# Performance work log

Hardware: AMD Instinct MI355X
Metric: run time of the kernel (lower is better)

Reference implementation:

```python
import jax, jax.numpy as jnp
import numpy as np

N, E, D, ED = 100000, 500000, 64, 32
MSG_IN = 4 * D + ED + 4  # 292


def _xavier(k, fi, fo):
    lim = np.sqrt(6.0 / (fi + fo)).astype(np.float32)
    return jax.random.uniform(k, (fi, fo), jnp.float32, -lim, lim)


def mlp(x, W1, b1, W2, b2):
    return jax.nn.gelu(x @ W1 + b1, approximate=False) @ W2 + b2


def layernorm(x, g, b, eps=1e-5):
    m = jnp.mean(x, -1, keepdims=True)
    v = jnp.mean((x - m) ** 2, -1, keepdims=True)
    return (x - m) / jnp.sqrt(v + eps) * g + b


def setup_inputs() -> dict:
    key = jax.random.key(0)
    ks = jax.random.split(key, 40)
    node_u = jax.random.normal(ks[0], (N, 5), jnp.float32)
    src = jax.random.randint(ks[1], (E,), 0, N)
    dst = jax.random.randint(ks[2], (E,), 0, N)
    edge_index = jnp.stack([src, dst], 0).astype(jnp.int64)
    dxy = jax.random.normal(ks[3], (E, 2), jnp.float32) * 0.01
    r = jnp.linalg.norm(dxy, axis=-1, keepdims=True)
    edge_attr = jnp.concatenate([dxy, r], -1)
    mean_mom = jax.random.normal(ks[4], (2,), jnp.float32)
    std_mom = jax.random.uniform(ks[5], (2,), jnp.float32) + 0.5
    edge_memory = jax.random.normal(ks[6], (E, D), jnp.float32) * 0.1
    p = {}
    # phi_node: 5->64->64
    p['pn_W1'] = _xavier(ks[7], 5, D); p['pn_b1'] = jnp.zeros((D,))
    p['pn_W2'] = _xavier(ks[8], D, D); p['pn_b2'] = jnp.zeros((D,))
    # input_proj: 5->64
    p['ip_W'] = _xavier(ks[9], 5, D); p['ip_b'] = jnp.zeros((D,))
    # phi_edge: 1->32->32
    p['pe_W1'] = _xavier(ks[10], 1, ED); p['pe_b1'] = jnp.zeros((ED,))
    p['pe_W2'] = _xavier(ks[11], ED, ED); p['pe_b2'] = jnp.zeros((ED,))
    # phi_msg: 292->128->64
    p['pm_W1'] = _xavier(ks[12], MSG_IN, 128); p['pm_b1'] = jnp.zeros((128,))
    p['pm_W2'] = _xavier(ks[13], 128, D); p['pm_b2'] = jnp.zeros((D,))
    # psi_rho: 64->64->1
    p['prho_W1'] = _xavier(ks[14], D, 64); p['prho_b1'] = jnp.zeros((64,))
    p['prho_W2'] = _xavier(ks[15], 64, 1); p['prho_b2'] = jnp.zeros((1,))
    # psi_e: 64->64->1
    p['pen_W1'] = _xavier(ks[16], D, 64); p['pen_b1'] = jnp.zeros((64,))
    p['pen_W2'] = _xavier(ks[17], 64, 1); p['pen_b2'] = jnp.zeros((1,))
    # psi_rhou: 64->64->2
    p['pmu_W1'] = _xavier(ks[18], D, 64); p['pmu_b1'] = jnp.zeros((64,))
    p['pmu_W2'] = _xavier(ks[19], 64, 2); p['pmu_b2'] = jnp.zeros((2,))
    # psi_visc: 64->32->1
    p['pv_W1'] = _xavier(ks[20], D, 32); p['pv_b1'] = jnp.zeros((32,))
    p['pv_W2'] = _xavier(ks[21], 32, 1); p['pv_b2'] = jnp.zeros((1,))
    p['ln_g'] = jnp.ones((D,)); p['ln_b'] = jnp.zeros((D,))
    return dict(node_u=node_u, edge_attr=edge_attr, mean_mom=mean_mom,
                std_mom=std_mom, edge_memory=edge_memory, edge_index=edge_index, **p)


def reference(node_u, edge_attr, mean_mom, std_mom, edge_memory,
              pn_W1, pn_b1, pn_W2, pn_b2, ip_W, ip_b,
              pe_W1, pe_b1, pe_W2, pe_b2, pm_W1, pm_b1, pm_W2, pm_b2,
              prho_W1, prho_b1, prho_W2, prho_b2, pen_W1, pen_b1, pen_W2, pen_b2,
              pmu_W1, pmu_b1, pmu_W2, pmu_b2, pv_W1, pv_b1, pv_W2, pv_b2,
              ln_g, ln_b, edge_index):
    src, dst = edge_index[0], edge_index[1]
    dx, dy, r = edge_attr[:, 0:1], edge_attr[:, 1:2], edge_attr[:, 2:3]
    n = jnp.concatenate([dx, dy], -1) / (r + 1e-12)            # (E,2) unit normals
    t = jnp.stack([-n[:, 1], n[:, 0]], axis=1)                 # (E,2) tangents
    # momentum projections in physical units
    rhou_phys = node_u[:, 3:5] * std_mom + mean_mom            # (N,2)
    rs, rd = rhou_phys[src], rhou_phys[dst]
    scale = jnp.linalg.norm(std_mom) + 1e-8
    vel_proj = jnp.concatenate([
        jnp.sum(rs * n, -1, keepdims=True), jnp.sum(rs * t, -1, keepdims=True),
        jnp.sum(rd * n, -1, keepdims=True), jnp.sum(rd * t, -1, keepdims=True)], -1) / scale
    # node embeddings with residual projection
    h = mlp(node_u, pn_W1, pn_b1, pn_W2, pn_b2) + node_u @ ip_W + ip_b
    h_src, h_dst = h[src], h[dst]
    eps = mlp(r, pe_W1, pe_b1, pe_W2, pe_b2)                   # (E,32)
    msg_in = jnp.concatenate([h_src, h_dst, h_src + h_dst,
                              (h_src - h_dst) ** 2, eps, vel_proj], -1)  # (E,292)
    m = mlp(msg_in, pm_W1, pm_b1, pm_W2, pm_b2)                # (E,64)
    m = layernorm(m + edge_memory, ln_g, ln_b)
    a_rho = mlp(m, prho_W1, prho_b1, prho_W2, prho_b2)[:, 0]
    a_e = mlp(m, pen_W1, pen_b1, pen_W2, pen_b2)[:, 0]
    a_rhou = mlp(m, pmu_W1, pmu_b1, pmu_W2, pmu_b2)            # (E,2)
    alpha = jax.nn.sigmoid(mlp(m, pv_W1, pv_b1, pv_W2, pv_b2)[:, 0])[:, None]
    du = node_u[dst] - node_u[src]
    F_rho = a_rho[:, None] * n - alpha * du[:, 0:1] * n
    F_e = a_e[:, None] * n - alpha * du[:, 1:2] * n
    F_rhou = a_rhou[:, 0:1] * n + a_rhou[:, 1:2] * t - alpha * du[:, 3:5]
    return (F_rho, F_e, F_rhou, n, r[:, 0], alpha[:, 0], m)
```

## Files before the change

kernel.cpp:

```cpp
#include <hip/hip_runtime.h>
#include <math.h>

#define NN 100000
#define NE 500000

typedef short bf16x8 __attribute__((ext_vector_type(8)));
typedef float f32x4 __attribute__((ext_vector_type(4)));
typedef float f32x16 __attribute__((ext_vector_type(16)));

__device__ __forceinline__ float gelu_f(float x) {
  const float t = x * x;
  const float p = fmaf(t, 0.10294325f, 2.3022084f);
  const float E = __builtin_amdgcn_exp2f(x * p);
  const float r = __builtin_amdgcn_rcpf(E + 1.0f);
  return fmaf(-x, r, x);
}
__device__ __forceinline__ unsigned cvtpk(float lo, float hi) {
  unsigned r;
  asm("v_cvt_pk_bf16_f32 %0, %1, %2" : "=v"(r) : "v"(lo), "v"(hi));
  return r;
}
__device__ __forceinline__ short f2bf(float x) { return (short)cvtpk(x, x); }
__device__ __forceinline__ unsigned pack2(float a, float b) { return cvtpk(a, b); }
__device__ __forceinline__ float bf2f(short s) {
  unsigned u = ((unsigned)(unsigned short)s) << 16;
  return __builtin_bit_cast(float, u);
}
__device__ __forceinline__ float bf2f_lo(unsigned w) {
  return __builtin_bit_cast(float, w << 16);
}
__device__ __forceinline__ float bf2f_hi(unsigned w) {
  return __builtin_bit_cast(float, w & 0xFFFF0000u);
}

#define MFMA16(a, b, c) __builtin_amdgcn_mfma_f32_16x16x32_bf16((a), (b), (c), 0, 0, 0)
#define MFMA32(a, b, c) __builtin_amdgcn_mfma_f32_32x32x16_bf16((a), (b), (c), 0, 0, 0)

__global__ __launch_bounds__(256) void node_h_kernel(
    const float* __restrict__ node_u,
    const float* __restrict__ b1, const float* __restrict__ b2,
    const float* __restrict__ ipb,
    const short* __restrict__ W1NP, const short* __restrict__ IPNP,
    const short* __restrict__ W2NP,
    unsigned short* __restrict__ h) {
  __shared__ float sU[64 * 5];
  __shared__ short sG[64 * 72];
  const int tid = threadIdx.x;
  const int lane = tid & 63;
  const int wv = tid >> 6;
  const int l31 = lane & 31, hi = lane >> 5;
  const int mt = wv & 1, nh = wv >> 1;
  const int n0 = blockIdx.x * 64;
  const int nrem = NN - n0;

  {
    const int cnt = (nrem < 64 ? nrem : 64) * 5;
    for (int t = tid; t < cnt; t += 256) sU[t] = node_u[(size_t)n0 * 5 + t];
  }
  __syncthreads();

  const int row_node = mt * 32 + l31;
  const int col = nh * 32 + l31;
  bf16x8 au;
#pragma unroll
  for (int e = 0; e < 8; ++e)
    au[e] = (hi == 0 && e < 5) ? f2bf(sU[row_node * 5 + e]) : (short)0;
  f32x16 acc1, accip;
  const float b1v = b1[col];
  const float ipv = ipb[col] + b2[col];
#pragma unroll
  for (int reg = 0; reg < 16; ++reg) { acc1[reg] = b1v; accip[reg] = ipv; }
  acc1 = MFMA32(au, *(const bf16x8*)(W1NP + nh * 512 + lane * 8), acc1);
  accip = MFMA32(au, *(const bf16x8*)(IPNP + nh * 512 + lane * 8), accip);
#pragma unroll
  for (int reg = 0; reg < 16; ++reg) {
    const int r = mt * 32 + (reg & 3) + 8 * (reg >> 2) + 4 * hi;
    sG[r * 72 + col] = f2bf(gelu_f(acc1[reg]));
  }
  __syncthreads();

  {
    const char* arow = (const char*)sG + row_node * 144 + hi * 16;
    const short* BW = W2NP + nh * 4 * 512 + lane * 8;
    f32x16 acc = accip;
#pragma unroll
    for (int ks = 0; ks < 4; ++ks)
      acc = MFMA32(*(const bf16x8*)(arow + ks * 32),
                   *(const bf16x8*)(BW + ks * 512), acc);
#pragma unroll
    for (int reg = 0; reg < 16; ++reg) {
      const int r = mt * 32 + (reg & 3) + 8 * (reg >> 2) + 4 * hi;
      const int node = n0 + r;
      if (node < NN) h[(size_t)node * 64 + col] = (unsigned short)f2bf(acc[reg]);
    }
  }
}

__global__ __launch_bounds__(256) void prep_kernel(
    const float* __restrict__ pm_W1, const float* __restrict__ pm_b1,
    const float* __restrict__ pm_W2,
    const float* __restrict__ prho_W1, const float* __restrict__ pen_W1,
    const float* __restrict__ pmu_W1, const float* __restrict__ pv_W1,
    const float* __restrict__ prho_b1, const float* __restrict__ pen_b1,
    const float* __restrict__ pmu_b1, const float* __restrict__ pv_b1,
    const float* __restrict__ pe_W2, const float* __restrict__ pe_b2,
    const float* __restrict__ prho_W2, const float* __restrict__ pen_W2,
    const float* __restrict__ pmu_W2, const float* __restrict__ pv_W2,
    const float* __restrict__ prho_b2, const float* __restrict__ pen_b2,
    const float* __restrict__ pmu_b2, const float* __restrict__ pv_b2,
    const float* __restrict__ pn_W1, const float* __restrict__ pn_W2,
    const float* __restrict__ ip_W,
    short* __restrict__ W1P, short* __restrict__ W2P, short* __restrict__ WHP,
    float* __restrict__ HB, short* __restrict__ WOP, float* __restrict__ HB2,
    float* __restrict__ B1F, short* __restrict__ W1NP, short* __restrict__ IPNP,
    short* __restrict__ W2NP) {
  int t = blockIdx.x * 256 + threadIdx.x;
  if (t < 30720) {
    const int nt = t / 7680, rem = t % 7680;
    const int ks = rem / 512, li = rem % 512;
    const int l = li >> 3, e = li & 7;
    const int k = ks * 16 + ((l >> 5) << 3) + e;
    const int n = nt * 32 + (l & 31);
    float v = 0.0f;
    if (k < 64) v = pm_W1[k * 128 + n] + pm_W1[(128 + k) * 128 + n];
    else if (k < 128) v = pm_W1[k * 128 + n] + pm_W1[(64 + k) * 128 + n];
    else if (k < 192) v = pm_W1[(64 + k) * 128 + n];
    else if (k < 224) {
      const int i = k - 192;
      for (int j = 0; j < 32; ++j) v += pe_W2[i * 32 + j] * pm_W1[(256 + j) * 128 + n];
    } else if (k < 228) v = pm_W1[(64 + k) * 128 + n];
    W1P[t] = f2bf(v);
    return;
  }
  t -= 30720;
  if (t < 8192) {
    const int nt = t / 2048, rem = t % 2048;
    const int ks = rem / 512, li = rem % 512;
    const int l = li >> 3, e = li & 7;
    const int k = ks * 32 + ((l >> 4) << 3) + e;
    const int n = nt * 16 + (l & 15);
    W2P[t] = f2bf(pm_W2[k * 64 + n]);
    return;
  }
  t -= 8192;
  if (t < 14336) {
    const int nt = t / 2048, rem = t % 2048;
    const int ks = rem / 512, li = rem % 512;
    const int l = li >> 3, e = li & 7;
    const int k = ks * 16 + ((l >> 5) << 3) + e;
    const int col = nt * 32 + (l & 31);
    float v;
    if (col < 64) v = prho_W1[k * 64 + col];
    else if (col < 128) v = pen_W1[k * 64 + (col - 64)];
    else if (col < 192) v = pmu_W1[k * 64 + (col - 128)];
    else v = pv_W1[k * 32 + (col - 192)];
    WHP[t] = f2bf(v);
    return;
  }
  t -= 14336;
  if (t < 224) {
    HB[t] = (t < 64) ? prho_b1[t]
          : (t < 128) ? pen_b1[t - 64]
          : (t < 192) ? pmu_b1[t - 128]
          : pv_b1[t - 192];
    return;
  }
  t -= 224;
  if (t < 3584) {
    const int ks = t / 512, li = t % 512;
    const int l = li >> 3, e = li & 7;
    const int k = ks * 32 + ((l >> 4) << 3) + e;
    const int j = l & 15;
    float v = 0.0f;
    if (j == 0 && k < 64) v = prho_W2[k];
    else if (j == 1 && k >= 64 && k < 128) v = pen_W2[k - 64];
    else if (j == 2 && k >= 128 && k < 192) v = pmu_W2[(k - 128) * 2 + 0];
    else if (j == 3 && k >= 128 && k < 192) v = pmu_W2[(k - 128) * 2 + 1];
    else if (j == 4 && k >= 192 && k < 224) v = pv_W2[k - 192];
    WOP[t] = f2bf(v);
    return;
  }
  t -= 3584;
  if (t < 16) {
    HB2[t] = (t == 0) ? prho_b2[0]
           : (t == 1) ? pen_b2[0]
           : (t == 2) ? pmu_b2[0]
           : (t == 3) ? pmu_b2[1]
           : (t == 4) ? pv_b2[0] : 0.0f;
    return;
  }
  t -= 16;
  if (t < 128) {
    float v = pm_b1[t];
    for (int j = 0; j < 32; ++j) v += pe_b2[j] * pm_W1[(256 + j) * 128 + t];
    B1F[t] = v;
    return;
  }
  t -= 128;
  if (t < 1024) {
    const int nt = t / 512, li = t % 512;
    const int l = li >> 3, e = li & 7;
    const int k = ((l >> 5) << 3) + e;
    const int n = nt * 32 + (l & 31);
    W1NP[t] = (k < 5) ? f2bf(pn_W1[k * 64 + n]) : (short)0;
    return;
  }
  t -= 1024;
  if (t < 1024) {
    const int nt = t / 512, li = t % 512;
    const int l = li >> 3, e = li & 7;
    const int k = ((l >> 5) << 3) + e;
    const int n = nt * 32 + (l & 31);
    IPNP[t] = (k < 5) ? f2bf(ip_W[k * 64 + n]) : (short)0;
    return;
  }
  t -= 1024;
  if (t < 4096) {
    const int nt = t / 2048, rem = t % 2048;
    const int ks = rem / 512, li = rem % 512;
    const int l = li >> 3, e = li & 7;
    const int k = ks * 16 + ((l >> 5) << 3) + e;
    const int n = nt * 32 + (l & 31);
    W2NP[t] = f2bf(pn_W2[k * 64 + n]);
  }
}

struct EdgeArgs {
  const float *node_u, *edge_attr, *mean_mom, *std_mom, *edge_mem;
  const int* eidx;
  const float *pe_W1, *pe_b1;
  const float *B1F, *pm_b2;
  const float *ln_g, *ln_b;
  const unsigned short* h;
  const short *W1P, *W2P, *WHP, *WOP;
  const float *HB, *HB2;
  float* out;
};

#define SMS 248
#define H1S 136
#define MSR 72
#define ZST 248

#define OFF_A    0
#define OFF_AM   15872
#define OFF_SC   20480
#define OFF_SC2  21504
#define OFF_PART 22528
#define SMEM_BYTES 23040

__global__ __launch_bounds__(256, 7) void edge_kernel(EdgeArgs A) {
  __shared__ __align__(16) char smem[SMEM_BYTES];
  short* aA = (short*)(smem + OFF_A);
  short* aZ = (short*)(smem + OFF_A);
  short* aH1 = (short*)(smem + OFF_A);
  short* aM = (short*)(smem + OFF_AM);
  float* sSc = (float*)(smem + OFF_SC);
  float* sSc2 = (float*)(smem + OFF_SC2);
  float2* sPart = (float2*)(smem + OFF_PART);

  const int tid = threadIdx.x;
  const int e0 = blockIdx.x * 32;
  const int lane = tid & 63;
  const int wv = tid >> 6;
  const int l15 = lane & 15, g = lane >> 4;
  const int l31 = lane & 31, hi = lane >> 5;
  const int mt = wv & 1, nh = wv >> 1;

  if (tid < 32) {
    const int e = e0 + tid;
    const int s = A.eidx[e];
    const int d = A.eidx[NE + e];
    const float dx = A.edge_attr[e * 3 + 0];
    const float dy = A.edge_attr[e * 3 + 1];
    const float r = A.edge_attr[e * 3 + 2];
    const float inv = 1.0f / (r + 1e-12f);
    const float n0 = dx * inv, n1 = dy * inv;
    const float* us = A.node_u + (size_t)s * 5;
    const float* ud = A.node_u + (size_t)d * 5;
    const float sm0 = A.std_mom[0], sm1 = A.std_mom[1];
    const float mm0 = A.mean_mom[0], mm1 = A.mean_mom[1];
    const float rs0 = fmaf(us[3], sm0, mm0), rs1 = fmaf(us[4], sm1, mm1);
    const float rd0 = fmaf(ud[3], sm0, mm0), rd1 = fmaf(ud[4], sm1, mm1);
    const float isc = 1.0f / (sqrtf(sm0 * sm0 + sm1 * sm1) + 1e-8f);
    unsigned* vp = (unsigned*)(aA + tid * SMS + 224);
    vp[0] = pack2((rs0 * n0 + rs1 * n1) * isc, (-rs0 * n1 + rs1 * n0) * isc);
    vp[1] = pack2((rd0 * n0 + rd1 * n1) * isc, (-rd0 * n1 + rd1 * n0) * isc);
    unsigned* zp = (unsigned*)(aA + tid * SMS + 228);
#pragma unroll
    for (int z = 0; z < 6; ++z) zp[z] = 0u;
    float* st = &sSc[tid * 8];
    st[0] = n0; st[1] = n1; st[2] = r;
    st[3] = ud[0] - us[0];
    st[4] = ud[1] - us[1];
    st[5] = ud[3] - us[3];
    st[6] = ud[4] - us[4];
  }
  {
    const int i = tid & 31, eg = tid >> 5;
    const float w1 = A.pe_W1[i], b1 = A.pe_b1[i];
#pragma unroll
    for (int p = 0; p < 4; ++p) {
      const int el = eg * 4 + p;
      const float rv = A.edge_attr[(e0 + el) * 3 + 2];
      aA[el * SMS + 192 + i] = f2bf(gelu_f(fmaf(rv, w1, b1)));
    }
  }
  {
    const int c = tid & 31, eg = tid >> 5;
    int si[4], di[4];
#pragma unroll
    for (int p = 0; p < 4; ++p) {
      si[p] = A.eidx[e0 + eg * 4 + p];
      di[p] = A.eidx[NE + e0 + eg * 4 + p];
    }
    unsigned usr[4], udr[4];
#pragma unroll
    for (int p = 0; p < 4; ++p) {
      usr[p] = ((const unsigned*)(A.h + (size_t)si[p] * 64))[c];
      udr[p] = ((const unsigned*)(A.h + (size_t)di[p] * 64))[c];
    }
#pragma unroll
    for (int p = 0; p < 4; ++p) {
      const int el = eg * 4 + p;
      unsigned* rp = (unsigned*)((char*)aA + el * (SMS * 2));
      rp[c] = usr[p];
      rp[32 + c] = udr[p];
      const float s0 = bf2f_lo(usr[p]), s1 = bf2f_hi(usr[p]);
      const float d0 = bf2f_lo(udr[p]), d1 = bf2f_hi(udr[p]);
      const float q0 = s0 - d0, q1 = s1 - d1;
      rp[64 + c] = pack2(q0 * q0, q1 * q1);
    }
  }
  __syncthreads();

  unsigned h1pk[8];
  {
    const char* arow = (const char*)aA + l31 * (SMS * 2) + hi * 16;
    const short* BW = A.W1P + wv * 15 * 512 + lane * 8;
    f32x16 acc = {0.f, 0.f, 0.f, 0.f, 0.f, 0.f, 0.f, 0.f,
                  0.f, 0.f, 0.f, 0.f, 0.f, 0.f, 0.f, 0.f};
    for (int ks = 0; ks < 15; ++ks) {
      acc = MFMA32(*(const bf16x8*)(arow + ks * 32),
                   *(const bf16x8*)(BW + ks * 512), acc);
    }
    const float bb = A.B1F[wv * 32 + l31];
#pragma unroll
    for (int r8 = 0; r8 < 8; ++r8)
      h1pk[r8] = pack2(gelu_f(acc[2 * r8] + bb), gelu_f(acc[2 * r8 + 1] + bb));
  }
  __syncthreads();

  {
    const int col = wv * 32 + l31;
#pragma unroll
    for (int r8 = 0; r8 < 8; ++r8) {
      const int reg = 2 * r8;
      const int row = (reg & 3) + 8 * (reg >> 2) + 4 * hi;
      aH1[row * H1S + col] = (short)h1pk[r8];
      aH1[(row + 1) * H1S + col] = (short)(h1pk[r8] >> 16);
    }
  }
  __syncthreads();

  {
    const int rb = mt * 16 + g * 4;
    const int c0 = (nh * 2 + 0) * 16 + l15, c1 = (nh * 2 + 1) * 16 + l15;
    float em0[4], em1[4];
#pragma unroll
    for (int rg = 0; rg < 4; ++rg) {
      em0[rg] = A.edge_mem[(size_t)(e0 + rb + rg) * 64 + c0];
      em1[rg] = A.edge_mem[(size_t)(e0 + rb + rg) * 64 + c1];
    }
    const char* arow = (const char*)aH1 + (mt * 16 + l15) * (H1S * 2) + g * 16;
    const short* BW = A.W2P + nh * 2 * 4 * 512 + lane * 8;
    f32x4 ac0 = {0.f, 0.f, 0.f, 0.f}, ac1 = ac0;
    for (int ks = 0; ks < 4; ++ks) {
      const bf16x8 a = *(const bf16x8*)(arow + ks * 64);
      ac0 = MFMA16(a, *(const bf16x8*)(BW + (0 * 4 + ks) * 512), ac0);
      ac1 = MFMA16(a, *(const bf16x8*)(BW + (1 * 4 + ks) * 512), ac1);
    }
    const float bb0 = A.pm_b2[c0], bb1 = A.pm_b2[c1];
#pragma unroll
    for (int rg = 0; rg < 4; ++rg) {
      const int row = rb + rg;
      const float x0 = ac0[rg] + bb0 + em0[rg];
      const float x1 = ac1[rg] + bb1 + em1[rg];
      const unsigned pk = pack2(x0, x1);
      aM[row * MSR + c0] = (short)pk;
      aM[row * MSR + c1] = (short)(pk >> 16);
      float sx = x0 + x1;
      float sq = fmaf(x0, x0, x1 * x1);
#pragma unroll
      for (int m = 1; m < 16; m <<= 1) {
        sx += __shfl_xor(sx, m, 64);
        sq += __shfl_xor(sq, m, 64);
      }
      if (l15 == 0) sPart[row * 2 + nh] = make_float2(sx, sq);
    }
  }
  __syncthreads();

  {
    const float lg = A.ln_g[lane], lb = A.ln_b[lane];
#pragma unroll
    for (int p = 0; p < 8; ++p) {
      const int r = p * 4 + wv;
      const float x = bf2f(aM[r * MSR + lane]);
      const float2 pa = sPart[r * 2 + 0], pb = sPart[r * 2 + 1];
      const float mean = (pa.x + pb.x) * (1.0f / 64.0f);
      const float var = fmaxf((pa.y + pb.y) * (1.0f / 64.0f) - mean * mean, 0.0f);
      const float rstd = rsqrtf(var + 1e-5f);
      const float y = fmaf((x - mean) * rstd, lg, lb);
      aM[r * MSR + lane] = f2bf(y);
    }
  }
  __syncthreads();

  {
    const char* arow = (const char*)aM + l31 * (MSR * 2) + hi * 16;
    bf16x8 af0 = *(const bf16x8*)(arow);
    bf16x8 af1 = *(const bf16x8*)(arow + 32);
    bf16x8 af2 = *(const bf16x8*)(arow + 64);
    bf16x8 af3 = *(const bf16x8*)(arow + 96);
    for (int nt = wv; nt < 7; nt += 4) {
      const short* BW = A.WHP + nt * 4 * 512 + lane * 8;
      f32x16 acc = {0.f, 0.f, 0.f, 0.f, 0.f, 0.f, 0.f, 0.f,
                    0.f, 0.f, 0.f, 0.f, 0.f, 0.f, 0.f, 0.f};
      acc = MFMA32(af0, *(const bf16x8*)(BW + 0 * 512), acc);
      acc = MFMA32(af1, *(const bf16x8*)(BW + 1 * 512), acc);
      acc = MFMA32(af2, *(const bf16x8*)(BW + 2 * 512), acc);
      acc = MFMA32(af3, *(const bf16x8*)(BW + 3 * 512), acc);
      const int col = nt * 32 + l31;
      const float bb = A.HB[col];
#pragma unroll
      for (int i = 0; i < 8; ++i) {
        const int reg = 2 * i;
        const int row = (reg & 3) + 8 * (reg >> 2) + 4 * hi;
        const unsigned pk = pack2(gelu_f(acc[reg] + bb), gelu_f(acc[reg + 1] + bb));
        aZ[row * ZST + col] = (short)pk;
        aZ[(row + 1) * ZST + col] = (short)(pk >> 16);
      }
    }
  }
  __syncthreads();

  if (wv < 2) {
    f32x4 acc = {0.f, 0.f, 0.f, 0.f};
    for (int ks = 0; ks < 7; ++ks) {
      const bf16x8 a = *(const bf16x8*)((const char*)aZ + (wv * 16 + l15) * (ZST * 2) + ks * 64 + g * 16);
      const bf16x8 b = *(const bf16x8*)(A.WOP + ks * 512 + lane * 8);
      acc = MFMA16(a, b, acc);
    }
    if (l15 < 5) {
      const float bb = A.HB2[l15];
#pragma unroll
      for (int rg = 0; rg < 4; ++rg)
        sSc2[(wv * 16 + g * 4 + rg) * 8 + l15] = acc[rg] + bb;
    }
    asm volatile("s_waitcnt lgkmcnt(0)" ::: "memory");
    __builtin_amdgcn_sched_barrier(0);
    if (lane < 16) {
      const int e = wv * 16 + lane;
      const float* st = &sSc[e * 8];
      const float n0 = st[0], n1 = st[1], r = st[2];
      const float du0 = st[3], du1 = st[4], du3 = st[5], du4 = st[6];
      const float arho = sSc2[e * 8 + 0], aen = sSc2[e * 8 + 1];
      const float amu0 = sSc2[e * 8 + 2], amu1 = sSc2[e * 8 + 3];
      const float av = sSc2[e * 8 + 4];
      const float alpha = __builtin_amdgcn_rcpf(1.0f + __builtin_amdgcn_exp2f(-1.4426950408f * av));
      const size_t ge = (size_t)(e0 + e);
      float* out = A.out;
      const float c0 = arho - alpha * du0;
      out[ge * 2 + 0] = c0 * n0;
      out[ge * 2 + 1] = c0 * n1;
      const float c1 = aen - alpha * du1;
      out[(size_t)2 * NE + ge * 2 + 0] = c1 * n0;
      out[(size_t)2 * NE + ge * 2 + 1] = c1 * n1;
      out[(size_t)4 * NE + ge * 2 + 0] = amu0 * n0 - amu1 * n1 - alpha * du3;
      out[(size_t)4 * NE + ge * 2 + 1] = amu0 * n1 + amu1 * n0 - alpha * du4;
      out[(size_t)6 * NE + ge * 2 + 0] = n0;
      out[(size_t)6 * NE + ge * 2 + 1] = n1;
      out[(size_t)8 * NE + ge] = r;
      out[(size_t)9 * NE + ge] = alpha;
    }
  } else {
    float* out_m = A.out + (size_t)10 * NE;
    const int rbase = (wv - 2) * 16;
#pragma unroll
    for (int rr = 0; rr < 16; ++rr) {
      const int row = rbase + rr;
      out_m[(size_t)(e0 + row) * 64 + lane] = bf2f(aM[row * MSR + lane]);
    }
  }
}

extern "C" void kernel_launch(void* const* d_in, const int* in_sizes, int n_in,
                              void* d_out, int out_size, void* d_ws, size_t ws_size,
                              hipStream_t stream) {
  char* ws = (char*)d_ws;
  unsigned short* h = (unsigned short*)ws;
  short* W1P  = (short*)(ws + 12800000);
  short* W2P  = (short*)(ws + 12861440);
  short* WHP  = (short*)(ws + 12877824);
  float* HB   = (float*)(ws + 12906496);
  short* WOP  = (short*)(ws + 12907392);
  float* HB2  = (float*)(ws + 12914560);
  float* B1F  = (float*)(ws + 12914624);
  short* W1NP = (short*)(ws + 12915136);
  short* IPNP = (short*)(ws + 12917184);
  short* W2NP = (short*)(ws + 12919232);

  EdgeArgs A;
  A.node_u = (const float*)d_in[0];
  A.edge_attr = (const float*)d_in[1];
  A.mean_mom = (const float*)d_in[2];
  A.std_mom = (const float*)d_in[3];
  A.edge_mem = (const float*)d_in[4];
  A.eidx = (const int*)d_in[5];
  A.pe_W1 = (const float*)d_in[12];
  A.pe_b1 = (const float*)d_in[13];
  A.B1F = B1F;
  A.pm_b2 = (const float*)d_in[19];
  A.ln_g = (const float*)d_in[36];
  A.ln_b = (const float*)d_in[37];
  A.h = h;
  A.W1P = W1P;
  A.W2P = W2P;
  A.WHP = WHP;
  A.WOP = WOP;
  A.HB = HB;
  A.HB2 = HB2;
  A.out = (float*)d_out;

  prep_kernel<<<248, 256, 0, stream>>>(
      (const float*)d_in[16], (const float*)d_in[17], (const float*)d_in[18],
      (const float*)d_in[20], (const float*)d_in[24],
      (const float*)d_in[28], (const float*)d_in[32],
      (const float*)d_in[21], (const float*)d_in[25],
      (const float*)d_in[29], (const float*)d_in[33],
      (const float*)d_in[14], (const float*)d_in[15],
      (const float*)d_in[22], (const float*)d_in[26],
      (const float*)d_in[30], (const float*)d_in[34],
      (const float*)d_in[23], (const float*)d_in[27],
      (const float*)d_in[31], (const float*)d_in[35],
      (const float*)d_in[6], (const float*)d_in[8], (const float*)d_in[10],
      W1P, W2P, WHP, HB, WOP, HB2, B1F, W1NP, IPNP, W2NP);
  node_h_kernel<<<(NN + 63) / 64, 256, 0, stream>>>(
      (const float*)d_in[0], (const float*)d_in[7], (const float*)d_in[9],
      (const float*)d_in[11], W1NP, IPNP, W2NP, h);
  edge_kernel<<<NE / 32, 256, 0, stream>>>(A);
}
```

Before: 185.0 us.

## Reload edge scalars in epilogue to shrink LDS and raise occupancy

Drops the per-edge scalar staging arrays in shared memory. In the output epilogue it reloads the edge indices, edge attributes and node_u values from global memory, issuing the loads before the final MFMA loop to hide their latency. The head outputs are placed in the unused padding of the aZ rows. This cuts LDS per block from 23040 to 20480 bytes, and launch bounds move from 7 to 8 blocks per CU. The cost is extra global gathers and recomputing the normal, plus more register pressure under the tighter launch bound.

```diff
diff --git a/kernel.cpp b/kernel.cpp
--- a/kernel.cpp
+++ b/kernel.cpp
@@ -244,19 +244,15 @@
 
 #define OFF_A    0
 #define OFF_AM   15872
-#define OFF_SC   20480
-#define OFF_SC2  21504
-#define OFF_PART 22528
-#define SMEM_BYTES 23040
-
-__global__ __launch_bounds__(256, 7) void edge_kernel(EdgeArgs A) {
+#define OFF_PART 8704
+#define SMEM_BYTES 20480
+
+__global__ __launch_bounds__(256, 8) void edge_kernel(EdgeArgs A) {
   __shared__ __align__(16) char smem[SMEM_BYTES];
   short* aA = (short*)(smem + OFF_A);
   short* aZ = (short*)(smem + OFF_A);
   short* aH1 = (short*)(smem + OFF_A);
   short* aM = (short*)(smem + OFF_AM);
-  float* sSc = (float*)(smem + OFF_SC);
-  float* sSc2 = (float*)(smem + OFF_SC2);
   float2* sPart = (float2*)(smem + OFF_PART);
 
   const int tid = threadIdx.x;
@@ -289,12 +285,6 @@
     unsigned* zp = (unsigned*)(aA + tid * SMS + 228);
 #pragma unroll
     for (int z = 0; z < 6; ++z) zp[z] = 0u;
-    float* st = &sSc[tid * 8];
-    st[0] = n0; st[1] = n1; st[2] = r;
-    st[3] = ud[0] - us[0];
-    st[4] = ud[1] - us[1];
-    st[5] = ud[3] - us[3];
-    st[6] = ud[4] - us[4];
   }
   {
     const int i = tid & 31, eg = tid >> 5;
@@ -446,6 +436,23 @@
   __syncthreads();
 
   if (wv < 2) {
+    const int e = wv * 16 + l15;
+    const size_t ge = (size_t)(e0 + e);
+    int s = 0, d = 0;
+    float dx = 0.f, dy = 0.f, rr = 0.f;
+    float u0s = 0.f, u1s = 0.f, u3s = 0.f, u4s = 0.f;
+    float u0d = 0.f, u1d = 0.f, u3d = 0.f, u4d = 0.f;
+    if (lane < 16) {
+      s = A.eidx[ge];
+      d = A.eidx[NE + ge];
+      dx = A.edge_attr[ge * 3 + 0];
+      dy = A.edge_attr[ge * 3 + 1];
+      rr = A.edge_attr[ge * 3 + 2];
+      const float* us = A.node_u + (size_t)s * 5;
+      const float* ud = A.node_u + (size_t)d * 5;
+      u0s = us[0]; u1s = us[1]; u3s = us[3]; u4s = us[4];
+      u0d = ud[0]; u1d = ud[1]; u3d = ud[3]; u4d = ud[4];
+    }
     f32x4 acc = {0.f, 0.f, 0.f, 0.f};
     for (int ks = 0; ks < 7; ++ks) {
       const bf16x8 a = *(const bf16x8*)((const char*)aZ + (wv * 16 + l15) * (ZST * 2) + ks * 64 + g * 16);
@@ -456,20 +463,20 @@
       const float bb = A.HB2[l15];
 #pragma unroll
       for (int rg = 0; rg < 4; ++rg)
-        sSc2[(wv * 16 + g * 4 + rg) * 8 + l15] = acc[rg] + bb;
+        *(float*)(smem + (size_t)(wv * 16 + g * 4 + rg) * 496 + 448 + l15 * 4) = acc[rg] + bb;
     }
     asm volatile("s_waitcnt lgkmcnt(0)" ::: "memory");
     __builtin_amdgcn_sched_barrier(0);
     if (lane < 16) {
-      const int e = wv * 16 + lane;
-      const float* st = &sSc[e * 8];
-      const float n0 = st[0], n1 = st[1], r = st[2];
-      const float du0 = st[3], du1 = st[4], du3 = st[5], du4 = st[6];
-      const float arho = sSc2[e * 8 + 0], aen = sSc2[e * 8 + 1];
-      const float amu0 = sSc2[e * 8 + 2], amu1 = sSc2[e * 8 + 3];
-      const float av = sSc2[e * 8 + 4];
+      const float inv = 1.0f / (rr + 1e-12f);
+      const float n0 = dx * inv, n1 = dy * inv;
+      const float du0 = u0d - u0s, du1 = u1d - u1s;
+      const float du3 = u3d - u3s, du4 = u4d - u4s;
+      const float* sc2 = (const float*)(smem + (size_t)e * 496 + 448);
+      const float arho = sc2[0], aen = sc2[1];
+      const float amu0 = sc2[2], amu1 = sc2[3];
+      const float av = sc2[4];
       const float alpha = __builtin_amdgcn_rcpf(1.0f + __builtin_amdgcn_exp2f(-1.4426950408f * av));
-      const size_t ge = (size_t)(e0 + e);
       float* out = A.out;
       const float c0 = arho - alpha * du0;
       out[ge * 2 + 0] = c0 * n0;
@@ -481,15 +488,15 @@
       out[(size_t)4 * NE + ge * 2 + 1] = amu0 * n1 + amu1 * n0 - alpha * du4;
       out[(size_t)6 * NE + ge * 2 + 0] = n0;
       out[(size_t)6 * NE + ge * 2 + 1] = n1;
-      out[(size_t)8 * NE + ge] = r;
+      out[(size_t)8 * NE + ge] = rr;
       out[(size_t)9 * NE + ge] = alpha;
     }
   } else {
     float* out_m = A.out + (size_t)10 * NE;
     const int rbase = (wv - 2) * 16;
 #pragma unroll
-    for (int rr = 0; rr < 16; ++rr) {
-      const int row = rbase + rr;
+    for (int rr2 = 0; rr2 < 16; ++rr2) {
+      const int row = rbase + rr2;
       out_m[(size_t)(e0 + row) * 64 + lane] = bf2f(aM[row * MSR + lane]);
     }
   }
```

After: 182.3 us. No clear change (-1.4%).
